# Kernel optimization log

Hardware: AMD Instinct MI355X
Metric: run time of the kernel (lower is better)

The kernel has to match this reference:

```python
import jax, jax.numpy as jnp
import numpy as np

BATCH_SIZE_PER_IM = 512
FG_FRACTION = 0.25
FG_THRESH = 0.5
BG_THRESH_HI = 0.5
BG_THRESH_LO = 0.0
MAX_FG = int(FG_FRACTION * BATCH_SIZE_PER_IM)  # 128


def _rand_boxes(key, shape):
    a = jax.random.uniform(key, shape + (4,), dtype=jnp.float32)
    ymin = jnp.minimum(a[..., 0], a[..., 2])
    ymax = jnp.maximum(a[..., 0], a[..., 2]) + 1e-3
    xmin = jnp.minimum(a[..., 1], a[..., 3])
    xmax = jnp.maximum(a[..., 1], a[..., 3]) + 1e-3
    return jnp.stack([ymin, xmin, ymax, xmax], axis=-1)


def setup_inputs() -> dict:
    key = jax.random.key(0)
    k1, k2, k3, k4 = jax.random.split(key, 4)
    B, N, G = 32, 8192, 128
    boxes = _rand_boxes(k1, (B, N))
    gt_boxes = _rand_boxes(k2, (B, G))
    gt_labels = jax.random.randint(k3, (B, G), 0, 91, dtype=jnp.int32)
    noise = jax.random.uniform(k4, (B, N + G), dtype=jnp.float32)
    return {"boxes": boxes, "gt_boxes": gt_boxes, "gt_labels": gt_labels, "noise": noise}


def _bbox_overlap(boxes, gt_boxes):
    # boxes: [B, M, 4], gt_boxes: [B, G, 4], layout (ymin, xmin, ymax, xmax)
    b_ymin, b_xmin, b_ymax, b_xmax = [boxes[..., i:i + 1] for i in range(4)]  # [B,M,1]
    g_ymin, g_xmin, g_ymax, g_xmax = [gt_boxes[..., i][:, None, :] for i in range(4)]  # [B,1,G]
    i_ymin = jnp.maximum(b_ymin, g_ymin)
    i_xmin = jnp.maximum(b_xmin, g_xmin)
    i_ymax = jnp.minimum(b_ymax, g_ymax)
    i_xmax = jnp.minimum(b_xmax, g_xmax)
    i_area = jnp.maximum(i_ymax - i_ymin, 0.0) * jnp.maximum(i_xmax - i_xmin, 0.0)  # [B,M,G]
    b_area = (b_ymax - b_ymin) * (b_xmax - b_xmin)           # [B,M,1]
    g_area = (g_ymax - g_ymin) * (g_xmax - g_xmin)           # [B,1,G]
    iou = i_area / (b_area + g_area - i_area)
    # padded gt boxes (filled with -1) get IoU = -1
    padding = jnp.logical_and(i_ymin < 0, i_xmin < 0)
    return jnp.where(padding, -1.0, iou)


def reference(boxes, gt_boxes, gt_labels, noise):
    boxes = jax.lax.stop_gradient(boxes)
    all_boxes = jnp.concatenate([boxes, gt_boxes], axis=1)        # [B, M=N+G, 4]
    iou = _bbox_overlap(all_boxes, gt_boxes)                      # [B, M, G]
    max_ov = jnp.max(iou, axis=2)                                 # [B, M]
    p2l = jnp.argmax(iou, axis=2).astype(jnp.int32)               # [B, M]
    box_t = jnp.take_along_axis(gt_boxes, p2l[..., None], axis=1)  # [B, M, 4]
    cls_t = jnp.take_along_axis(gt_labels, p2l, axis=1)           # [B, M]
    pos = max_ov > FG_THRESH
    neg = jnp.logical_and(max_ov >= BG_THRESH_LO, max_ov < BG_THRESH_HI)
    cls_t = jnp.where(neg, 0, cls_t)
    box_t = jnp.where(neg[..., None], 0.0, box_t)
    p2l = jnp.where(neg, 0, p2l)
    # --- balanced fg/bg subsampling (random scores provided in `noise`) ---
    pos_score = jnp.where(pos, noise, -1.0)
    kth = jax.lax.top_k(pos_score, MAX_FG)[0][:, -1:]             # [B,1] threshold
    sel_pos = jnp.logical_and(pos, pos_score >= kth)              # at most MAX_FG fg
    # selected fg get priority band 2+, bg band [0,1), rest -1
    combined = jnp.where(sel_pos, 2.0 + noise, jnp.where(neg, noise, -1.0))
    _, idx = jax.lax.top_k(combined, BATCH_SIZE_PER_IM)           # [B, K]
    rois = jnp.take_along_axis(all_boxes, idx[..., None], axis=1)      # [B, K, 4]
    sample_box_t = jnp.take_along_axis(box_t, idx[..., None], axis=1)  # [B, K, 4]
    sample_cls_t = jnp.take_along_axis(cls_t, idx, axis=1)             # [B, K]
    sample_p2l = jnp.take_along_axis(p2l, idx, axis=1)                 # [B, K]
    return sample_box_t, sample_cls_t, rois, sample_p2l
```

## Files before the change

kernel.cpp:

```cpp
#include <hip/hip_runtime.h>
#include <stdint.h>

#define BATCH 32
#define NBOX 8192
#define NGT 128
#define M (NBOX + NGT)
#define K_OUT 512
#define MAX_FG 128
#define C_CAP 256
#define S_CAP 256
#define U_CAP 1024

#define IOU_TPB 256
#define IOU_VPT 2
#define IOU_SPAN (IOU_TPB * IOU_VPT)
#define IOU_BPB ((M + IOU_SPAN - 1) / IOU_SPAN)

__device__ __forceinline__ unsigned int bkt1024(float ns) {
    unsigned int u = (unsigned int)(ns * 16777216.0f) >> 14;
    return u > 1023u ? 1023u : u;
}

__global__ __launch_bounds__(256) void iou_kernel(
    const float* __restrict__ boxes,
    const float* __restrict__ gt_boxes,
    unsigned short* __restrict__ packed)
{
    const int b   = blockIdx.x / IOU_BPB;
    const int blk = blockIdx.x % IOU_BPB;
    const int t   = threadIdx.x;

    __shared__ float4 sgt[NGT];
    __shared__ float  sga[NGT];
    if (t < NGT) {
        float4 g = ((const float4*)gt_boxes)[b * NGT + t];
        sgt[t] = g;
        sga[t] = __fmul_rn(__fsub_rn(g.z, g.x), __fsub_rn(g.w, g.y));
    }
    __syncthreads();

    const int m0 = blk * IOU_SPAN + t;
    const int m1 = m0 + IOU_TPB;
    const bool v0 = m0 < M, v1 = m1 < M;

    float4 bb0 = make_float4(0.f, 0.f, 1.f, 1.f);
    float4 bb1 = make_float4(0.f, 0.f, 1.f, 1.f);
    if (v0) bb0 = (m0 < NBOX) ? ((const float4*)boxes)[b * NBOX + m0] : sgt[m0 - NBOX];
    if (v1) bb1 = (m1 < NBOX) ? ((const float4*)boxes)[b * NBOX + m1] : sgt[m1 - NBOX];
    float a0 = __fmul_rn(__fsub_rn(bb0.z, bb0.x), __fsub_rn(bb0.w, bb0.y));
    float a1 = __fmul_rn(__fsub_rn(bb1.z, bb1.x), __fsub_rn(bb1.w, bb1.y));

    float best0 = -1e30f, best1 = -1e30f;
    int i0 = 0, i1 = 0;
    #pragma unroll 4
    for (int g = 0; g < NGT; ++g) {
        float4 gg = sgt[g];
        float  ga = sga[g];
        {
            float iymin = fmaxf(bb0.x, gg.x);
            float ixmin = fmaxf(bb0.y, gg.y);
            float iymax = fminf(bb0.z, gg.z);
            float ixmax = fminf(bb0.w, gg.w);
            float ia  = __fmul_rn(fmaxf(__fsub_rn(iymax, iymin), 0.0f),
                                  fmaxf(__fsub_rn(ixmax, ixmin), 0.0f));
            float den = __fsub_rn(__fadd_rn(a0, ga), ia);
            float iou = __fdiv_rn(ia, den);
            if (iou > best0) { best0 = iou; i0 = g; }
        }
        {
            float iymin = fmaxf(bb1.x, gg.x);
            float ixmin = fmaxf(bb1.y, gg.y);
            float iymax = fminf(bb1.z, gg.z);
            float ixmax = fminf(bb1.w, gg.w);
            float ia  = __fmul_rn(fmaxf(__fsub_rn(iymax, iymin), 0.0f),
                                  fmaxf(__fsub_rn(ixmax, ixmin), 0.0f));
            float den = __fsub_rn(__fadd_rn(a1, ga), ia);
            float iou = __fdiv_rn(ia, den);
            if (iou > best1) { best1 = iou; i1 = g; }
        }
    }
    if (v0) {
        bool pos = best0 > 0.5f;
        bool neg = (best0 >= 0.0f) && (best0 < 0.5f);
        packed[b * M + m0] = (unsigned short)(i0 | (neg ? 256 : 0) | (pos ? 512 : 0));
    }
    if (v1) {
        bool pos = best1 > 0.5f;
        bool neg = (best1 >= 0.0f) && (best1 < 0.5f);
        packed[b * M + m1] = (unsigned short)(i1 | (neg ? 256 : 0) | (pos ? 512 : 0));
    }
}

__global__ __launch_bounds__(1024) void select_kernel(
    const float* __restrict__ boxes,
    const float* __restrict__ gt_boxes,
    const int*   __restrict__ gt_labels,
    const float* __restrict__ noise,
    const unsigned short* __restrict__ packed,
    float* __restrict__ out)
{
    const int b = blockIdx.x;
    const int tid = threadIdx.x;

    __shared__ float sh_ns[M];
    __shared__ unsigned int hist[1024];
    __shared__ unsigned int hist2[1024];
    __shared__ unsigned int bctr[1024];
    __shared__ unsigned char posmask[M / 8];
    __shared__ unsigned char negmask[M / 8];
    __shared__ float4 sgt[NGT];
    __shared__ int slab[NGT];
    __shared__ float C[C_CAP];
    __shared__ __align__(16) unsigned int   skey[S_CAP + 4];
    __shared__ __align__(16) unsigned short sm[S_CAP + 4];
    __shared__ unsigned int   ukey[U_CAP];
    __shared__ unsigned short um[U_CAP];
    __shared__ unsigned int sh_Bp, sh_needp, sh_cc, sh_n1a, sh_B, sh_kth;

    float* out_bt  = out;
    float* out_cls = out + BATCH * K_OUT * 4;
    float* out_roi = out + BATCH * K_OUT * 5;
    float* out_p2l = out + BATCH * K_OUT * 9;

    hist[tid] = 0;
    hist2[tid] = 0;
    bctr[tid] = 0;
    if (tid == 0) { sh_cc = 0; sh_n1a = 0; sh_B = 0; sh_kth = 0xBF800000u; }
    if (tid < NGT) {
        sgt[tid]  = ((const float4*)gt_boxes)[b * NGT + tid];
        slab[tid] = gt_labels[b * NGT + tid];
    }
    __syncthreads();

    float f[8];
    unsigned int pb = 0, nb = 0;
    {
        const uint4*  pk4 = (const uint4*)(packed + (size_t)b * M);
        const float4* ns4 = (const float4*)(noise + (size_t)b * M);
        {
            uint4 pv = pk4[tid];
            float4 n0 = ns4[2 * tid], n1v = ns4[2 * tid + 1];
            ((float4*)sh_ns)[2 * tid] = n0;
            ((float4*)sh_ns)[2 * tid + 1] = n1v;
            f[0] = n0.x; f[1] = n0.y; f[2] = n0.z; f[3] = n0.w;
            f[4] = n1v.x; f[5] = n1v.y; f[6] = n1v.z; f[7] = n1v.w;
            unsigned short e[8];
            e[0] = (unsigned short)(pv.x & 0xFFFF); e[1] = (unsigned short)(pv.x >> 16);
            e[2] = (unsigned short)(pv.y & 0xFFFF); e[3] = (unsigned short)(pv.y >> 16);
            e[4] = (unsigned short)(pv.z & 0xFFFF); e[5] = (unsigned short)(pv.z >> 16);
            e[6] = (unsigned short)(pv.w & 0xFFFF); e[7] = (unsigned short)(pv.w >> 16);
            #pragma unroll
            for (int k = 0; k < 8; ++k) {
                if (e[k] & 512) {
                    pb |= (1u << k);
                    atomicAdd(&hist2[bkt1024(f[k])], 1u);
                } else if (e[k] & 256) {
                    nb |= (1u << k);
                    atomicAdd(&hist[bkt1024(f[k])], 1u);
                }
            }
            posmask[tid] = (unsigned char)pb;
            negmask[tid] = (unsigned char)nb;
        }
        if (tid < 16) {
            int c = 1024 + tid;
            uint4 pv = pk4[c];
            float4 n0 = ns4[2 * c], n1v = ns4[2 * c + 1];
            ((float4*)sh_ns)[2 * c] = n0;
            ((float4*)sh_ns)[2 * c + 1] = n1v;
            float ft[8] = {n0.x, n0.y, n0.z, n0.w, n1v.x, n1v.y, n1v.z, n1v.w};
            unsigned short e[8];
            e[0] = (unsigned short)(pv.x & 0xFFFF); e[1] = (unsigned short)(pv.x >> 16);
            e[2] = (unsigned short)(pv.y & 0xFFFF); e[3] = (unsigned short)(pv.y >> 16);
            e[4] = (unsigned short)(pv.z & 0xFFFF); e[5] = (unsigned short)(pv.z >> 16);
            e[6] = (unsigned short)(pv.w & 0xFFFF); e[7] = (unsigned short)(pv.w >> 16);
            unsigned int pb2 = 0, nb2 = 0;
            #pragma unroll
            for (int k = 0; k < 8; ++k) {
                if (e[k] & 512) {
                    pb2 |= (1u << k);
                    atomicAdd(&hist2[bkt1024(ft[k])], 1u);
                } else if (e[k] & 256) {
                    nb2 |= (1u << k);
                    atomicAdd(&hist[bkt1024(ft[k])], 1u);
                }
            }
            posmask[c] = (unsigned char)pb2;
            negmask[c] = (unsigned char)nb2;
        }
    }
    __syncthreads();

    {
        const int wv = tid >> 6, ln = tid & 63;
        if (wv < 2) {
            unsigned int* H = wv ? hist2 : hist;
            unsigned int s[16];
            #pragma unroll
            for (int k = 0; k < 16; ++k) {
                unsigned int v = H[k * 64 + ln];
                #pragma unroll
                for (int off = 1; off < 64; off <<= 1) {
                    unsigned int o = __shfl_down(v, off, 64);
                    if (ln + off < 64) v += o;
                }
                s[k] = v;
            }
            unsigned int after = 0;
            #pragma unroll
            for (int k = 15; k >= 0; --k) {
                unsigned int tot = __shfl(s[k], 0, 64);
                H[k * 64 + ln] = s[k] + after;
                after += tot;
            }
        }
    }
    __syncthreads();
    const unsigned int nneg = hist[0];
    const unsigned int npos = hist2[0];

    if (npos >= MAX_FG) {
        {
            unsigned int S  = hist2[tid];
            unsigned int Sn = (tid < 1023) ? hist2[tid + 1] : 0;
            if (S >= MAX_FG && Sn < MAX_FG) { sh_Bp = tid; sh_needp = MAX_FG - Sn; }
        }
        __syncthreads();
        const unsigned int Bp = sh_Bp, needp = sh_needp;
        #pragma unroll
        for (int k = 0; k < 8; ++k) {
            if (((pb >> k) & 1u) && bkt1024(f[k]) == Bp) {
                unsigned int slot = atomicAdd(&sh_cc, 1u);
                if (slot < C_CAP) C[slot] = f[k];
            }
        }
        if (tid < 16) {
            unsigned int pb2 = posmask[1024 + tid];
            #pragma unroll
            for (int k = 0; k < 8; ++k) {
                if ((pb2 >> k) & 1u) {
                    float v = sh_ns[(1024 + tid) * 8 + k];
                    if (bkt1024(v) == Bp) {
                        unsigned int slot = atomicAdd(&sh_cc, 1u);
                        if (slot < C_CAP) C[slot] = v;
                    }
                }
            }
        }
        __syncthreads();
        {
            unsigned int cc = min(sh_cc, (unsigned int)C_CAP);
            if (tid < (int)cc) {
                float my = C[tid];
                unsigned int g = 0, e = 0;
                for (unsigned int j = 0; j < cc; ++j) {
                    float v = C[j];
                    g += (v > my) ? 1u : 0u;
                    e += (v == my) ? 1u : 0u;
                }
                if (g < needp && g + e >= needp) sh_kth = __float_as_uint(my);
            }
        }
        __syncthreads();
    }
    const float kthf = __uint_as_float(sh_kth);

    #pragma unroll
    for (int k = 0; k < 8; ++k) {
        if (((pb >> k) & 1u) && f[k] >= kthf) {
            unsigned int slot = atomicAdd(&sh_n1a, 1u);
            if (slot < S_CAP) {
                skey[slot] = __float_as_uint(__fadd_rn(2.0f, f[k]));
                sm[slot]   = (unsigned short)(tid * 8 + k);
            }
        }
    }
    if (tid < 16) {
        unsigned int pb2 = posmask[1024 + tid];
        #pragma unroll
        for (int k = 0; k < 8; ++k) {
            if ((pb2 >> k) & 1u) {
                int m = (1024 + tid) * 8 + k;
                float v = sh_ns[m];
                if (v >= kthf) {
                    unsigned int slot = atomicAdd(&sh_n1a, 1u);
                    if (slot < S_CAP) {
                        skey[slot] = __float_as_uint(__fadd_rn(2.0f, v));
                        sm[slot]   = (unsigned short)m;
                    }
                }
            }
        }
    }
    __syncthreads();
    const unsigned int n1 = min(sh_n1a, (unsigned int)S_CAP);
    const unsigned int k2 = K_OUT - n1;
    const bool enough_neg = (nneg >= k2);

    if (tid < 4) { skey[n1 + tid] = 0u; sm[n1 + tid] = 0xFFFFu; }
    if (enough_neg) {
        unsigned int S  = hist[tid];
        unsigned int Sn = (tid < 1023) ? hist[tid + 1] : 0;
        if (S >= k2 && Sn < k2) sh_B = tid;
    }
    __syncthreads();
    const unsigned int B1 = sh_B;

    if (tid < (int)n1) {
        unsigned int   ki = skey[tid];
        unsigned short mi = sm[tid];
        unsigned int r = 0;
        for (unsigned int j = 0; j < n1; j += 4) {
            uint4   kv = *(const uint4*)&skey[j];
            ushort4 mv = *(const ushort4*)&sm[j];
            r += (kv.x > ki || (kv.x == ki && mv.x < mi)) ? 1u : 0u;
            r += (kv.y > ki || (kv.y == ki && mv.y < mi)) ? 1u : 0u;
            r += (kv.z > ki || (kv.z == ki && mv.z < mi)) ? 1u : 0u;
            r += (kv.w > ki || (kv.w == ki && mv.w < mi)) ? 1u : 0u;
        }
        int mi_ = mi;
        int pkv = packed[(size_t)b * M + mi_];
        int lbl = pkv & 127;
        float4 roi = (mi_ < NBOX) ? ((const float4*)boxes)[b * NBOX + mi_]
                                  : sgt[mi_ - NBOX];
        ((float4*)out_bt)[b * K_OUT + r] = sgt[lbl];
        out_cls[b * K_OUT + r] = (float)slab[lbl];
        ((float4*)out_roi)[b * K_OUT + r] = roi;
        out_p2l[b * K_OUT + r] = (float)lbl;
    }

    #pragma unroll
    for (int k = 0; k < 8; ++k) {
        if ((nb >> k) & 1u) {
            float v = f[k];
            unsigned int be = bkt1024(v);
            if (be >= B1) {
                unsigned int base = (be < 1023) ? hist[be + 1] : 0;
                unsigned int a = base + atomicAdd(&bctr[be], 1u);
                if (a < U_CAP) {
                    ukey[a] = __float_as_uint(v);
                    um[a]   = (unsigned short)(tid * 8 + k);
                }
            }
        }
    }
    if (tid < 16) {
        unsigned int nb2 = negmask[1024 + tid];
        #pragma unroll
        for (int k = 0; k < 8; ++k) {
            if ((nb2 >> k) & 1u) {
                int m = (1024 + tid) * 8 + k;
                float v = sh_ns[m];
                unsigned int be = bkt1024(v);
                if (be >= B1) {
                    unsigned int base = (be < 1023) ? hist[be + 1] : 0;
                    unsigned int a = base + atomicAdd(&bctr[be], 1u);
                    if (a < U_CAP) {
                        ukey[a] = __float_as_uint(v);
                        um[a]   = (unsigned short)m;
                    }
                }
            }
        }
    }
    __syncthreads();

    const unsigned int q = min(hist[B1], (unsigned int)U_CAP);
    for (unsigned int a = tid; a < q; a += 1024) {
        unsigned int   ki = ukey[a];
        unsigned short mi = um[a];
        unsigned int be = bkt1024(__uint_as_float(ki));
        unsigned int base = (be < 1023) ? hist[be + 1] : 0;
        unsigned int end  = min(hist[be], q);
        unsigned int r = base;
        for (unsigned int j = base; j < end; ++j) {
            unsigned int kj = ukey[j];
            if (kj > ki || (kj == ki && um[j] < mi)) ++r;
        }
        if (r < k2) {
            float4 roi = (mi < NBOX) ? ((const float4*)boxes)[b * NBOX + mi]
                                     : sgt[mi - NBOX];
            unsigned int gr = n1 + r;
            ((float4*)out_bt)[b * K_OUT + gr] = make_float4(0.f, 0.f, 0.f, 0.f);
            out_cls[b * K_OUT + gr] = 0.0f;
            ((float4*)out_roi)[b * K_OUT + gr] = roi;
            out_p2l[b * K_OUT + gr] = 0.0f;
        }
    }

    if (!enough_neg) {
        __syncthreads();
        const unsigned int k3 = k2 - nneg;
        for (int m = tid; m < M; m += 1024) {
            if (((posmask[m >> 3] >> (m & 7)) & 1) && sh_ns[m] < kthf) {
                unsigned int r = 0;
                for (int m2 = 0; m2 < m; ++m2)
                    if (((posmask[m2 >> 3] >> (m2 & 7)) & 1) && sh_ns[m2] < kthf) ++r;
                if (r < k3) {
                    int pkv = packed[(size_t)b * M + m];
                    int lbl = pkv & 127;
                    float4 roi = (m < NBOX) ? ((const float4*)boxes)[b * NBOX + m]
                                            : sgt[m - NBOX];
                    unsigned int gr = n1 + nneg + r;
                    ((float4*)out_bt)[b * K_OUT + gr] = sgt[lbl];
                    out_cls[b * K_OUT + gr] = (float)slab[lbl];
                    ((float4*)out_roi)[b * K_OUT + gr] = roi;
                    out_p2l[b * K_OUT + gr] = (float)lbl;
                }
            }
        }
    }
}

extern "C" void kernel_launch(void* const* d_in, const int* in_sizes, int n_in,
                              void* d_out, int out_size, void* d_ws, size_t ws_size,
                              hipStream_t stream) {
    const float* boxes     = (const float*)d_in[0];
    const float* gt_boxes  = (const float*)d_in[1];
    const int*   gt_labels = (const int*)d_in[2];
    const float* noise     = (const float*)d_in[3];
    unsigned short* packed = (unsigned short*)d_ws;
    float* out = (float*)d_out;

    iou_kernel<<<BATCH * IOU_BPB, IOU_TPB, 0, stream>>>(boxes, gt_boxes, packed);
    select_kernel<<<BATCH, 1024, 0, stream>>>(boxes, gt_boxes, gt_labels, noise,
                                              packed, out);
}
```

Before: 115.9 us.

## Split IoU over GT halves and merge packed argmax keys in select kernel

The IoU kernel now splits the 128 GT boxes into two halves across separate blocks, with one box per thread instead of two, which raises block count and parallelism. Each half writes a 64-bit key (IoU bits high, inverted index low) so the select kernel can merge the halves with a max and keep the first-index tie-break. The select kernel decodes the pos/neg flags from the float bits and caches the argmax index in shared memory, replacing later global reads of the packed array. In exchange, intermediate traffic grows from 2 bytes to 16 bytes per box, and the loss of per-thread ILP may offset the gain.

Result: faster. 107.2 us (-7.5%).

```diff
diff --git a/kernel.cpp b/kernel.cpp
--- a/kernel.cpp
+++ b/kernel.cpp
@@ -11,84 +11,62 @@
 #define S_CAP 256
 #define U_CAP 1024
 
+#define GSPLIT 2
+#define GPER (NGT / GSPLIT)
 #define IOU_TPB 256
-#define IOU_VPT 2
-#define IOU_SPAN (IOU_TPB * IOU_VPT)
-#define IOU_BPB ((M + IOU_SPAN - 1) / IOU_SPAN)
+#define IOU_CB ((M + IOU_TPB - 1) / IOU_TPB)
 
 __device__ __forceinline__ unsigned int bkt1024(float ns) {
     unsigned int u = (unsigned int)(ns * 16777216.0f) >> 14;
     return u > 1023u ? 1023u : u;
 }
 
+#define U64KEY(lo, hi) (((unsigned long long)(hi) << 32) | (unsigned long long)(lo))
+
 __global__ __launch_bounds__(256) void iou_kernel(
     const float* __restrict__ boxes,
     const float* __restrict__ gt_boxes,
-    unsigned short* __restrict__ packed)
+    unsigned long long* __restrict__ part)
 {
-    const int b   = blockIdx.x / IOU_BPB;
-    const int blk = blockIdx.x % IOU_BPB;
-    const int t   = threadIdx.x;
-
-    __shared__ float4 sgt[NGT];
-    __shared__ float  sga[NGT];
-    if (t < NGT) {
-        float4 g = ((const float4*)gt_boxes)[b * NGT + t];
+    const int s  = blockIdx.x % GSPLIT;
+    const int cb = (blockIdx.x / GSPLIT) % IOU_CB;
+    const int b  = blockIdx.x / (GSPLIT * IOU_CB);
+    const int t  = threadIdx.x;
+    const int g0 = s * GPER;
+
+    __shared__ float4 sgt[GPER];
+    __shared__ float  sga[GPER];
+    if (t < GPER) {
+        float4 g = ((const float4*)gt_boxes)[b * NGT + g0 + t];
         sgt[t] = g;
         sga[t] = __fmul_rn(__fsub_rn(g.z, g.x), __fsub_rn(g.w, g.y));
     }
     __syncthreads();
 
-    const int m0 = blk * IOU_SPAN + t;
-    const int m1 = m0 + IOU_TPB;
-    const bool v0 = m0 < M, v1 = m1 < M;
-
-    float4 bb0 = make_float4(0.f, 0.f, 1.f, 1.f);
-    float4 bb1 = make_float4(0.f, 0.f, 1.f, 1.f);
-    if (v0) bb0 = (m0 < NBOX) ? ((const float4*)boxes)[b * NBOX + m0] : sgt[m0 - NBOX];
-    if (v1) bb1 = (m1 < NBOX) ? ((const float4*)boxes)[b * NBOX + m1] : sgt[m1 - NBOX];
-    float a0 = __fmul_rn(__fsub_rn(bb0.z, bb0.x), __fsub_rn(bb0.w, bb0.y));
-    float a1 = __fmul_rn(__fsub_rn(bb1.z, bb1.x), __fsub_rn(bb1.w, bb1.y));
-
-    float best0 = -1e30f, best1 = -1e30f;
-    int i0 = 0, i1 = 0;
+    const int m = cb * IOU_TPB + t;
+    if (m >= M) return;
+
+    float4 bb = (m < NBOX) ? ((const float4*)boxes)[b * NBOX + m]
+                           : ((const float4*)gt_boxes)[b * NGT + (m - NBOX)];
+    float ba = __fmul_rn(__fsub_rn(bb.z, bb.x), __fsub_rn(bb.w, bb.y));
+
+    float best = -1e30f;
+    int bi = 0;
     #pragma unroll 4
-    for (int g = 0; g < NGT; ++g) {
+    for (int g = 0; g < GPER; ++g) {
         float4 gg = sgt[g];
-        float  ga = sga[g];
-        {
-            float iymin = fmaxf(bb0.x, gg.x);
-            float ixmin = fmaxf(bb0.y, gg.y);
-            float iymax = fminf(bb0.z, gg.z);
-            float ixmax = fminf(bb0.w, gg.w);
-            float ia  = __fmul_rn(fmaxf(__fsub_rn(iymax, iymin), 0.0f),
-                                  fmaxf(__fsub_rn(ixmax, ixmin), 0.0f));
-            float den = __fsub_rn(__fadd_rn(a0, ga), ia);
-            float iou = __fdiv_rn(ia, den);
-            if (iou > best0) { best0 = iou; i0 = g; }
-        }
-        {
-            float iymin = fmaxf(bb1.x, gg.x);
-            float ixmin = fmaxf(bb1.y, gg.y);
-            float iymax = fminf(bb1.z, gg.z);
-            float ixmax = fminf(bb1.w, gg.w);
-            float ia  = __fmul_rn(fmaxf(__fsub_rn(iymax, iymin), 0.0f),
-                                  fmaxf(__fsub_rn(ixmax, ixmin), 0.0f));
-            float den = __fsub_rn(__fadd_rn(a1, ga), ia);
-            float iou = __fdiv_rn(ia, den);
-            if (iou > best1) { best1 = iou; i1 = g; }
-        }
-    }
-    if (v0) {
-        bool pos = best0 > 0.5f;
-        bool neg = (best0 >= 0.0f) && (best0 < 0.5f);
-        packed[b * M + m0] = (unsigned short)(i0 | (neg ? 256 : 0) | (pos ? 512 : 0));
-    }
-    if (v1) {
-        bool pos = best1 > 0.5f;
-        bool neg = (best1 >= 0.0f) && (best1 < 0.5f);
-        packed[b * M + m1] = (unsigned short)(i1 | (neg ? 256 : 0) | (pos ? 512 : 0));
-    }
+        float iymin = fmaxf(bb.x, gg.x);
+        float ixmin = fmaxf(bb.y, gg.y);
+        float iymax = fminf(bb.z, gg.z);
+        float ixmax = fminf(bb.w, gg.w);
+        float ia  = __fmul_rn(fmaxf(__fsub_rn(iymax, iymin), 0.0f),
+                              fmaxf(__fsub_rn(ixmax, ixmin), 0.0f));
+        float den = __fsub_rn(__fadd_rn(ba, sga[g]), ia);
+        float iou = __fdiv_rn(ia, den);
+        if (iou > best) { best = iou; bi = g0 + g; }
+    }
+    part[((size_t)s * BATCH + b) * M + m] =
+        U64KEY(127u - (unsigned int)bi, __float_as_uint(best));
 }
 
 __global__ __launch_bounds__(1024) void select_kernel(
@@ -96,13 +74,14 @@
     const float* __restrict__ gt_boxes,
     const int*   __restrict__ gt_labels,
     const float* __restrict__ noise,
-    const unsigned short* __restrict__ packed,
+    const unsigned long long* __restrict__ part,
     float* __restrict__ out)
 {
     const int b = blockIdx.x;
     const int tid = threadIdx.x;
 
     __shared__ float sh_ns[M];
+    __shared__ unsigned char sh_idx[M];
     __shared__ unsigned int hist[1024];
     __shared__ unsigned int hist2[1024];
     __shared__ unsigned int bctr[1024];
@@ -135,52 +114,76 @@
     float f[8];
     unsigned int pb = 0, nb = 0;
     {
-        const uint4*  pk4 = (const uint4*)(packed + (size_t)b * M);
+        const unsigned long long* P0 = part + ((size_t)0 * BATCH + b) * M;
+        const unsigned long long* P1 = part + ((size_t)1 * BATCH + b) * M;
         const float4* ns4 = (const float4*)(noise + (size_t)b * M);
         {
-            uint4 pv = pk4[tid];
-            float4 n0 = ns4[2 * tid], n1v = ns4[2 * tid + 1];
-            ((float4*)sh_ns)[2 * tid] = n0;
-            ((float4*)sh_ns)[2 * tid + 1] = n1v;
+            const int c = tid;
+            const uint4* a4 = (const uint4*)(P0 + (size_t)c * 8);
+            const uint4* b4 = (const uint4*)(P1 + (size_t)c * 8);
+            uint4 A0 = a4[0], A1 = a4[1], A2 = a4[2], A3 = a4[3];
+            uint4 B0 = b4[0], B1 = b4[1], B2 = b4[2], B3 = b4[3];
+            float4 n0 = ns4[2 * c], n1v = ns4[2 * c + 1];
+            ((float4*)sh_ns)[2 * c] = n0;
+            ((float4*)sh_ns)[2 * c + 1] = n1v;
             f[0] = n0.x; f[1] = n0.y; f[2] = n0.z; f[3] = n0.w;
             f[4] = n1v.x; f[5] = n1v.y; f[6] = n1v.z; f[7] = n1v.w;
-            unsigned short e[8];
-            e[0] = (unsigned short)(pv.x & 0xFFFF); e[1] = (unsigned short)(pv.x >> 16);
-            e[2] = (unsigned short)(pv.y & 0xFFFF); e[3] = (unsigned short)(pv.y >> 16);
-            e[4] = (unsigned short)(pv.z & 0xFFFF); e[5] = (unsigned short)(pv.z >> 16);
-            e[6] = (unsigned short)(pv.w & 0xFFFF); e[7] = (unsigned short)(pv.w >> 16);
+            unsigned long long ka[8] = {
+                U64KEY(A0.x, A0.y), U64KEY(A0.z, A0.w),
+                U64KEY(A1.x, A1.y), U64KEY(A1.z, A1.w),
+                U64KEY(A2.x, A2.y), U64KEY(A2.z, A2.w),
+                U64KEY(A3.x, A3.y), U64KEY(A3.z, A3.w)};
+            unsigned long long kb[8] = {
+                U64KEY(B0.x, B0.y), U64KEY(B0.z, B0.w),
+                U64KEY(B1.x, B1.y), U64KEY(B1.z, B1.w),
+                U64KEY(B2.x, B2.y), U64KEY(B2.z, B2.w),
+                U64KEY(B3.x, B3.y), U64KEY(B3.z, B3.w)};
             #pragma unroll
             for (int k = 0; k < 8; ++k) {
-                if (e[k] & 512) {
+                unsigned long long kk = ka[k] > kb[k] ? ka[k] : kb[k];
+                unsigned int ub = (unsigned int)(kk >> 32);
+                sh_idx[c * 8 + k] = (unsigned char)(127u - ((unsigned int)kk & 127u));
+                if (ub > 0x3F000000u) {
                     pb |= (1u << k);
                     atomicAdd(&hist2[bkt1024(f[k])], 1u);
-                } else if (e[k] & 256) {
+                } else if (ub < 0x3F000000u) {
                     nb |= (1u << k);
                     atomicAdd(&hist[bkt1024(f[k])], 1u);
                 }
             }
-            posmask[tid] = (unsigned char)pb;
-            negmask[tid] = (unsigned char)nb;
+            posmask[c] = (unsigned char)pb;
+            negmask[c] = (unsigned char)nb;
         }
         if (tid < 16) {
-            int c = 1024 + tid;
-            uint4 pv = pk4[c];
+            const int c = 1024 + tid;
+            const uint4* a4 = (const uint4*)(P0 + (size_t)c * 8);
+            const uint4* b4 = (const uint4*)(P1 + (size_t)c * 8);
+            uint4 A0 = a4[0], A1 = a4[1], A2 = a4[2], A3 = a4[3];
+            uint4 B0 = b4[0], B1 = b4[1], B2 = b4[2], B3 = b4[3];
             float4 n0 = ns4[2 * c], n1v = ns4[2 * c + 1];
             ((float4*)sh_ns)[2 * c] = n0;
             ((float4*)sh_ns)[2 * c + 1] = n1v;
             float ft[8] = {n0.x, n0.y, n0.z, n0.w, n1v.x, n1v.y, n1v.z, n1v.w};
-            unsigned short e[8];
-            e[0] = (unsigned short)(pv.x & 0xFFFF); e[1] = (unsigned short)(pv.x >> 16);
-            e[2] = (unsigned short)(pv.y & 0xFFFF); e[3] = (unsigned short)(pv.y >> 16);
-            e[4] = (unsigned short)(pv.z & 0xFFFF); e[5] = (unsigned short)(pv.z >> 16);
-            e[6] = (unsigned short)(pv.w & 0xFFFF); e[7] = (unsigned short)(pv.w >> 16);
+            unsigned long long ka[8] = {
+                U64KEY(A0.x, A0.y), U64KEY(A0.z, A0.w),
+                U64KEY(A1.x, A1.y), U64KEY(A1.z, A1.w),
+                U64KEY(A2.x, A2.y), U64KEY(A2.z, A2.w),
+                U64KEY(A3.x, A3.y), U64KEY(A3.z, A3.w)};
+            unsigned long long kb[8] = {
+                U64KEY(B0.x, B0.y), U64KEY(B0.z, B0.w),
+                U64KEY(B1.x, B1.y), U64KEY(B1.z, B1.w),
+                U64KEY(B2.x, B2.y), U64KEY(B2.z, B2.w),
+                U64KEY(B3.x, B3.y), U64KEY(B3.z, B3.w)};
             unsigned int pb2 = 0, nb2 = 0;
             #pragma unroll
             for (int k = 0; k < 8; ++k) {
-                if (e[k] & 512) {
+                unsigned long long kk = ka[k] > kb[k] ? ka[k] : kb[k];
+                unsigned int ub = (unsigned int)(kk >> 32);
+                sh_idx[c * 8 + k] = (unsigned char)(127u - ((unsigned int)kk & 127u));
+                if (ub > 0x3F000000u) {
                     pb2 |= (1u << k);
                     atomicAdd(&hist2[bkt1024(ft[k])], 1u);
-                } else if (e[k] & 256) {
+                } else if (ub < 0x3F000000u) {
                     nb2 |= (1u << k);
                     atomicAdd(&hist[bkt1024(ft[k])], 1u);
                 }
@@ -319,8 +322,7 @@
             r += (kv.w > ki || (kv.w == ki && mv.w < mi)) ? 1u : 0u;
         }
         int mi_ = mi;
-        int pkv = packed[(size_t)b * M + mi_];
-        int lbl = pkv & 127;
+        int lbl = sh_idx[mi_];
         float4 roi = (mi_ < NBOX) ? ((const float4*)boxes)[b * NBOX + mi_]
                                   : sgt[mi_ - NBOX];
         ((float4*)out_bt)[b * K_OUT + r] = sgt[lbl];
@@ -397,8 +399,7 @@
                 for (int m2 = 0; m2 < m; ++m2)
                     if (((posmask[m2 >> 3] >> (m2 & 7)) & 1) && sh_ns[m2] < kthf) ++r;
                 if (r < k3) {
-                    int pkv = packed[(size_t)b * M + m];
-                    int lbl = pkv & 127;
+                    int lbl = sh_idx[m];
                     float4 roi = (m < NBOX) ? ((const float4*)boxes)[b * NBOX + m]
                                             : sgt[m - NBOX];
                     unsigned int gr = n1 + nneg + r;
@@ -419,10 +420,10 @@
     const float* gt_boxes  = (const float*)d_in[1];
     const int*   gt_labels = (const int*)d_in[2];
     const float* noise     = (const float*)d_in[3];
-    unsigned short* packed = (unsigned short*)d_ws;
+    unsigned long long* part = (unsigned long long*)d_ws;
     float* out = (float*)d_out;
 
-    iou_kernel<<<BATCH * IOU_BPB, IOU_TPB, 0, stream>>>(boxes, gt_boxes, packed);
+    iou_kernel<<<BATCH * IOU_CB * GSPLIT, IOU_TPB, 0, stream>>>(boxes, gt_boxes, part);
     select_kernel<<<BATCH, 1024, 0, stream>>>(boxes, gt_boxes, gt_labels, noise,
-                                              packed, out);
+                                              part, out);
 }
```
